# Kernel optimization log

Hardware: AMD Instinct MI355X
Metric: run time of the kernel (lower is better)

The kernel has to match this reference:

```python
import jax, jax.numpy as jnp
import numpy as np

OUT_FEATURES = 11008
IN_FEATURES = 4096
GROUP_SIZE = 128
N_GROUPS = IN_FEATURES // GROUP_SIZE


def setup_inputs() -> dict:
    key = jax.random.key(0)
    k1, k2, k3 = jax.random.split(key, 3)
    x = jax.random.normal(k1, (4, 2048, IN_FEATURES), dtype=jnp.float32)
    # random packed bytes: every uint8 pattern decodes to a valid (low, high) nibble pair
    weight_packed = jax.random.randint(k2, (OUT_FEATURES, IN_FEATURES // 2), 0, 256, dtype=jnp.int32)
    # positive per-group scales (typical magnitude ~ max|w|/7)
    scales = jax.random.uniform(k3, (OUT_FEATURES, N_GROUPS), dtype=jnp.float32, minval=1e-3, maxval=0.05)
    return {"x": x, "weight_packed": weight_packed, "scales": scales}


def _dequant(weight_packed, scales):
    # unpack nibbles: low nibble = even index, high nibble = odd index; stored as (q+8)
    even = (weight_packed & 15) - 8                    # [O, I/2]
    odd = ((weight_packed >> 4) & 15) - 8              # [O, I/2]
    w_q = jnp.stack([even, odd], axis=-1).reshape(OUT_FEATURES, IN_FEATURES)  # interleave
    w = w_q.astype(jnp.float32).reshape(OUT_FEATURES, N_GROUPS, GROUP_SIZE)
    w = w * scales[:, :, None]                          # group-wise dequant
    return w.reshape(OUT_FEATURES, IN_FEATURES)


def reference(x, weight_packed, scales):
    w = _dequant(weight_packed, scales).astype(x.dtype)  # [O, I]
    # F.linear(x, w) = x @ w.T
    return jnp.einsum('bsi,oi->bso', x, w)
```

## Files before the change

### kernel.cpp

```cpp
#include <hip/hip_runtime.h>
#include <stdint.h>

#define K_DIM 4096
#define N_GROUPS 32

#define BM 128
#define BN 128
#define BK 32

typedef __attribute__((ext_vector_type(4))) float f32x4;
typedef __attribute__((ext_vector_type(8))) __bf16 bf16x8;

__device__ __forceinline__ unsigned short f2bf(float f) {
    union { float f; unsigned u; } c; c.f = f;
    unsigned u = c.u;
    u += 0x7FFFu + ((u >> 16) & 1u);
    return (unsigned short)(u >> 16);
}

__global__ __launch_bounds__(256) void cvt_x(const float* __restrict__ x,
                                             unsigned short* __restrict__ xb,
                                             int total) {
    int i = (blockIdx.x * 256 + threadIdx.x) * 8;
    if (i >= total) return;
    f32x4 a = *(const f32x4*)(x + i);
    f32x4 b = *(const f32x4*)(x + i + 4);
    union { unsigned short u[8]; uint4 v; } o;
    o.u[0] = f2bf(a.x); o.u[1] = f2bf(a.y); o.u[2] = f2bf(a.z); o.u[3] = f2bf(a.w);
    o.u[4] = f2bf(b.x); o.u[5] = f2bf(b.y); o.u[6] = f2bf(b.z); o.u[7] = f2bf(b.w);
    *(uint4*)(xb + i) = o.v;
}

__global__ __launch_bounds__(256) void dequant_w(const int* __restrict__ wp,
                                                 const float* __restrict__ sc,
                                                 unsigned short* __restrict__ wd,
                                                 int total4) {
    int idx = blockIdx.x * 256 + threadIdx.x;
    if (idx >= total4) return;
    const int4 v = ((const int4*)wp)[idx];
    int flat = idx << 2;
    int n = flat >> 11;
    int ci = flat & 2047;
    float s = sc[(n << 5) + (ci >> 6)];
    union { unsigned short u[8]; uint4 q; } o;
    int vv[4] = { v.x, v.y, v.z, v.w };
#pragma unroll
    for (int j = 0; j < 4; ++j) {
        int e = (vv[j] & 15) - 8;
        int d = ((vv[j] >> 4) & 15) - 8;
        o.u[2 * j]     = f2bf((float)e * s);
        o.u[2 * j + 1] = f2bf((float)d * s);
    }
    *(uint4*)(wd + ((size_t)n << 12) + (ci << 1)) = o.q;
}

__device__ __forceinline__ void gld16(const void* g, void* l) {
    __builtin_amdgcn_global_load_lds((__attribute__((address_space(1))) void*)g,
                                     (__attribute__((address_space(3))) void*)l,
                                     16, 0, 0);
}

__global__ __launch_bounds__(256, 2) void gemm_bt(const unsigned short* __restrict__ A,
                                                  const unsigned short* __restrict__ B,
                                                  float* __restrict__ C,
                                                  int M, int N) {
    __shared__ __align__(16) unsigned short As[2][BM * BK];
    __shared__ __align__(16) unsigned short Bs[2][BN * BK];

    const int tid  = threadIdx.x;
    const int wave = tid >> 6;
    const int lane = tid & 63;

    const int ntn = N / BN;
    const int G = 16;
    const int bpg = G * ntn;
    const int bid = blockIdx.x;
    const int g   = bid / bpg;
    const int r   = bid % bpg;
    const int tm  = g * G + (r & (G - 1));
    const int tn  = r >> 4;

    const int m0 = tm * BM;
    const int n0 = tn * BN;
    const int wm = (wave >> 1) * 64;
    const int wn = (wave & 1) * 64;

    const int srow = wave * 32 + (lane >> 2);
    const int scol = (lane & 3) * 8;
    const unsigned short* ag = A + (size_t)(m0 + srow) * K_DIM + scol;
    const unsigned short* bg = B + (size_t)(n0 + srow) * K_DIM + scol;
    const int lbase = wave * 1024;

    const int fr = lane & 15;
    const int fk = (lane >> 4) * 8;

    f32x4 acc[4][4] = {};

    gld16(ag, As[0] + lbase);
    gld16(ag + (size_t)16 * K_DIM, As[0] + lbase + 512);
    gld16(bg, Bs[0] + lbase);
    gld16(bg + (size_t)16 * K_DIM, Bs[0] + lbase + 512);

    int buf = 0;
    for (int k0 = 0; k0 < K_DIM; k0 += BK, buf ^= 1) {
        __syncthreads();

        if (k0 + BK < K_DIM) {
            const int kn = k0 + BK;
            unsigned short* al = As[buf ^ 1] + lbase;
            unsigned short* bl = Bs[buf ^ 1] + lbase;
            gld16(ag + kn, al);
            gld16(ag + kn + (size_t)16 * K_DIM, al + 512);
            gld16(bg + kn, bl);
            gld16(bg + kn + (size_t)16 * K_DIM, bl + 512);
        }

        const unsigned short* Ab = As[buf];
        const unsigned short* Bb = Bs[buf];
        bf16x8 af[4], bf[4];
#pragma unroll
        for (int i = 0; i < 4; ++i) {
            af[i] = *(const bf16x8*)(Ab + (wm + i * 16 + fr) * BK + fk);
            bf[i] = *(const bf16x8*)(Bb + (wn + i * 16 + fr) * BK + fk);
        }
#pragma unroll
        for (int i = 0; i < 4; ++i)
#pragma unroll
            for (int j = 0; j < 4; ++j)
                acc[i][j] = __builtin_amdgcn_mfma_f32_16x16x32_bf16(af[i], bf[j], acc[i][j], 0, 0, 0);
    }

    const int cr = (lane >> 4) * 4;
    const int cc = lane & 15;
#pragma unroll
    for (int i = 0; i < 4; ++i) {
#pragma unroll
        for (int j = 0; j < 4; ++j) {
            float* cp = C + (size_t)(m0 + wm + i * 16 + cr) * N + (n0 + wn + j * 16 + cc);
            cp[0]            = acc[i][j].x;
            cp[(size_t)N]    = acc[i][j].y;
            cp[(size_t)N*2]  = acc[i][j].z;
            cp[(size_t)N*3]  = acc[i][j].w;
        }
    }
}

__global__ __launch_bounds__(256, 2) void fused_gemm(const float* __restrict__ X,
                                                     const int* __restrict__ Wp,
                                                     const float* __restrict__ Sc,
                                                     float* __restrict__ C,
                                                     int M, int N) {
    __shared__ __align__(16) unsigned short As[BM * BK];
    __shared__ __align__(16) unsigned short Bs[BN * BK];

    const int tid  = threadIdx.x;
    const int wave = tid >> 6;
    const int lane = tid & 63;
    const int m0 = blockIdx.y * BM;
    const int n0 = blockIdx.x * BN;
    const int wm = (wave >> 1) * 64;
    const int wn = (wave & 1) * 64;

    const int fr = lane & 15;
    const int fk = (lane >> 4) * 8;

    f32x4 acc[4][4] = {};

    for (int k0 = 0; k0 < K_DIM; k0 += BK) {
        __syncthreads();
#pragma unroll
        for (int j = 0; j < 4; ++j) {
            int f = tid + 256 * j;
            int row = f >> 3, c4 = f & 7;
            f32x4 a = *(const f32x4*)(X + (size_t)(m0 + row) * K_DIM + k0 + c4 * 4);
            union { unsigned short u[4]; uint2 q; } o;
            o.u[0] = f2bf(a.x); o.u[1] = f2bf(a.y); o.u[2] = f2bf(a.z); o.u[3] = f2bf(a.w);
            *(uint2*)(As + row * BK + c4 * 4) = o.q;
        }
#pragma unroll
        for (int j = 0; j < 2; ++j) {
            int g = tid + 256 * j;
            int row = g >> 2, c4 = g & 3;
            const int4 v = *(const int4*)(Wp + (size_t)(n0 + row) * (K_DIM / 2) + (k0 >> 1) + c4 * 4);
            float s = Sc[(n0 + row) * N_GROUPS + (k0 >> 7)];
            union { unsigned short u[8]; uint4 q; } o;
            int vv[4] = { v.x, v.y, v.z, v.w };
#pragma unroll
            for (int t = 0; t < 4; ++t) {
                o.u[2 * t]     = f2bf((float)((vv[t] & 15) - 8) * s);
                o.u[2 * t + 1] = f2bf((float)(((vv[t] >> 4) & 15) - 8) * s);
            }
            *(uint4*)(Bs + row * BK + c4 * 8) = o.q;
        }
        __syncthreads();

        bf16x8 af[4], bf[4];
#pragma unroll
        for (int i = 0; i < 4; ++i) {
            af[i] = *(const bf16x8*)(As + (wm + i * 16 + fr) * BK + fk);
            bf[i] = *(const bf16x8*)(Bs + (wn + i * 16 + fr) * BK + fk);
        }
#pragma unroll
        for (int i = 0; i < 4; ++i)
#pragma unroll
            for (int j = 0; j < 4; ++j)
                acc[i][j] = __builtin_amdgcn_mfma_f32_16x16x32_bf16(af[i], bf[j], acc[i][j], 0, 0, 0);
    }

    const int cr = (lane >> 4) * 4;
    const int cc = lane & 15;
#pragma unroll
    for (int i = 0; i < 4; ++i) {
#pragma unroll
        for (int j = 0; j < 4; ++j) {
            float* cp = C + (size_t)(m0 + wm + i * 16 + cr) * N + (n0 + wn + j * 16 + cc);
            cp[0]           = acc[i][j].x;
            cp[(size_t)N]   = acc[i][j].y;
            cp[(size_t)N*2] = acc[i][j].z;
            cp[(size_t)N*3] = acc[i][j].w;
        }
    }
}

extern "C" void kernel_launch(void* const* d_in, const int* in_sizes, int n_in,
                              void* d_out, int out_size, void* d_ws, size_t ws_size,
                              hipStream_t stream) {
    const float* x  = (const float*)d_in[0];
    const int*   wp = (const int*)d_in[1];
    const float* sc = (const float*)d_in[2];
    float* out = (float*)d_out;

    const int M = in_sizes[0] / K_DIM;
    const int N = in_sizes[2] / N_GROUPS;

    const size_t xb_bytes = (size_t)M * K_DIM * 2;
    const size_t wd_bytes = (size_t)N * K_DIM * 2;

    if (ws_size >= xb_bytes + wd_bytes) {
        unsigned short* xb = (unsigned short*)d_ws;
        unsigned short* wd = (unsigned short*)((char*)d_ws + xb_bytes);
        int xtot = M * K_DIM;
        cvt_x<<<xtot / (256 * 8), 256, 0, stream>>>(x, xb, xtot);
        int wtot4 = N * (K_DIM / 2) / 4;
        dequant_w<<<(wtot4 + 255) / 256, 256, 0, stream>>>(wp, sc, wd, wtot4);
        gemm_bt<<<(M / BM) * (N / BN), 256, 0, stream>>>(xb, wd, out, M, N);
    } else {
        dim3 grid(N / BN, M / BM);
        fused_gemm<<<grid, 256, 0, stream>>>(x, wp, sc, out, M, N);
    }
}
```

Measured before the change: 1.313 ms.

## Replace bf16 GEMM with 256x256 eight-wave pipelined kernel with swizzled LDS

```diff
diff --git a/kernel.cpp b/kernel.cpp
--- a/kernel.cpp
+++ b/kernel.cpp
@@ -8,8 +8,14 @@
 #define BN 128
 #define BK 32
 
+#define BM8 256
+#define BN8 256
+#define BK8 64
+#define NT8 (K_DIM / BK8)
+
 typedef __attribute__((ext_vector_type(4))) float f32x4;
 typedef __attribute__((ext_vector_type(8))) __bf16 bf16x8;
+typedef __attribute__((ext_vector_type(4))) unsigned int u32x4;
 
 __device__ __forceinline__ unsigned short f2bf(float f) {
     union { float f; unsigned u; } c; c.f = f;
@@ -60,87 +66,158 @@
                                      16, 0, 0);
 }
 
-__global__ __launch_bounds__(256, 2) void gemm_bt(const unsigned short* __restrict__ A,
-                                                  const unsigned short* __restrict__ B,
-                                                  float* __restrict__ C,
-                                                  int M, int N) {
-    __shared__ __align__(16) unsigned short As[2][BM * BK];
-    __shared__ __align__(16) unsigned short Bs[2][BN * BK];
+__device__ __forceinline__ bf16x8 dsr(unsigned a) {
+    u32x4 d;
+    asm volatile("ds_read_b128 %0, %1" : "=v"(d) : "v"(a));
+    union { u32x4 u; bf16x8 b; } c; c.u = d;
+    return c.b;
+}
+
+__device__ __forceinline__ unsigned lds_addr(const void* p) {
+    return (unsigned)(uintptr_t)(__attribute__((address_space(3))) const void*)p;
+}
+
+#define MFMA_(va, vb, vc) __builtin_amdgcn_mfma_f32_16x16x32_bf16(va, vb, vc, 0, 0, 0)
+
+#define STAGE(regbase, g, k) do {                                   \
+    gld16((g) + (k), (regbase));                                    \
+    gld16((g) + (size_t)128 * K_DIM + (k), (regbase) + 4096); } while (0)
+
+__global__ __launch_bounds__(512, 2) void gemm8p(const unsigned short* __restrict__ A,
+                                                 const unsigned short* __restrict__ B,
+                                                 float* __restrict__ C,
+                                                 int M, int N) {
+    __shared__ __align__(16) unsigned short lds[2][4][8192];
 
     const int tid  = threadIdx.x;
     const int wave = tid >> 6;
     const int lane = tid & 63;
-
-    const int ntn = N / BN;
-    const int G = 16;
-    const int bpg = G * ntn;
+    const int wm = wave >> 2;
+    const int wn = wave & 3;
+
+    const int nwg = gridDim.x;
     const int bid = blockIdx.x;
-    const int g   = bid / bpg;
-    const int r   = bid % bpg;
-    const int tm  = g * G + (r & (G - 1));
-    const int tn  = r >> 4;
-
-    const int m0 = tm * BM;
-    const int n0 = tn * BN;
-    const int wm = (wave >> 1) * 64;
-    const int wn = (wave & 1) * 64;
-
-    const int srow = wave * 32 + (lane >> 2);
-    const int scol = (lane & 3) * 8;
-    const unsigned short* ag = A + (size_t)(m0 + srow) * K_DIM + scol;
-    const unsigned short* bg = B + (size_t)(n0 + srow) * K_DIM + scol;
-    const int lbase = wave * 1024;
+    const int q = nwg >> 3, r7 = nwg & 7;
+    const int xcd = bid & 7, loc = bid >> 3;
+    const int tile = (xcd < r7 ? xcd * (q + 1) : r7 * (q + 1) + (xcd - r7) * q) + loc;
+    const int ntm = M / BM8;
+    const int tm = tile % ntm;
+    const int tn = tile / ntm;
+    const int m0 = tm * BM8;
+    const int n0 = tn * BN8;
+
+    const int srow = lane >> 2;
+    const int sx   = ((lane & 3) * 8) ^ (((lane >> 3) & 3) << 3);
+    const unsigned short* Ag = A + (size_t)(m0 + wave * 16 + srow) * K_DIM + sx;
+    const unsigned short* Bg = B + (size_t)(n0 + wave * 16 + srow) * K_DIM + sx;
+    unsigned short* L  = &lds[0][0][0];
+    unsigned short* Ld = L + wave * 512;
 
     const int fr = lane & 15;
-    const int fk = (lane >> 4) * 8;
-
-    f32x4 acc[4][4] = {};
-
-    gld16(ag, As[0] + lbase);
-    gld16(ag + (size_t)16 * K_DIM, As[0] + lbase + 512);
-    gld16(bg, Bs[0] + lbase);
-    gld16(bg + (size_t)16 * K_DIM, Bs[0] + lbase + 512);
-
-    int buf = 0;
-    for (int k0 = 0; k0 < K_DIM; k0 += BK, buf ^= 1) {
-        __syncthreads();
-
-        if (k0 + BK < K_DIM) {
-            const int kn = k0 + BK;
-            unsigned short* al = As[buf ^ 1] + lbase;
-            unsigned short* bl = Bs[buf ^ 1] + lbase;
-            gld16(ag + kn, al);
-            gld16(ag + kn + (size_t)16 * K_DIM, al + 512);
-            gld16(bg + kn, bl);
-            gld16(bg + kn + (size_t)16 * K_DIM, bl + 512);
-        }
-
-        const unsigned short* Ab = As[buf];
-        const unsigned short* Bb = Bs[buf];
-        bf16x8 af[4], bf[4];
-#pragma unroll
-        for (int i = 0; i < 4; ++i) {
-            af[i] = *(const bf16x8*)(Ab + (wm + i * 16 + fr) * BK + fk);
-            bf[i] = *(const bf16x8*)(Bb + (wn + i * 16 + fr) * BK + fk);
-        }
-#pragma unroll
-        for (int i = 0; i < 4; ++i)
-#pragma unroll
-            for (int j = 0; j < 4; ++j)
-                acc[i][j] = __builtin_amdgcn_mfma_f32_16x16x32_bf16(af[i], bf[j], acc[i][j], 0, 0, 0);
+    const unsigned rofs = (unsigned)(fr * 64 + (((lane >> 4) * 16) ^ (((fr >> 1) & 3) << 4)));
+    const unsigned ldsb = lds_addr(L);
+    const unsigned aoff = ldsb + (unsigned)(wm * 8192) + rofs;
+    const unsigned boff = ldsb + 32768u + (unsigned)(wn * 4096) + rofs;
+
+    f32x4 acc[8][4] = {};
+    bf16x8 a0[4], a1[4], b0[4], b1[4];
+
+    STAGE(Ld + 0 * 8192, Ag, 0);
+    STAGE(Ld + 1 * 8192, Ag, 32);
+    STAGE(Ld + 2 * 8192, Bg, 0);
+    STAGE(Ld + 3 * 8192, Bg, 32);
+    STAGE(Ld + 32768 + 2 * 8192, Bg, 64);
+    STAGE(Ld + 32768 + 0 * 8192, Ag, 64);
+    STAGE(Ld + 32768 + 3 * 8192, Bg, 96);
+    asm volatile("s_waitcnt vmcnt(6)" ::: "memory");
+    __builtin_amdgcn_s_barrier();
+
+    for (int T = 0; T < NT8; ++T) {
+        const int buf = T & 1;
+        const unsigned ab = aoff + (unsigned)(buf * 65536);
+        const unsigned bb = boff + (unsigned)(buf * 65536);
+        unsigned short* Lc = Ld + buf * 32768;
+        unsigned short* Ln = Ld + (buf ^ 1) * 32768;
+        const int kn1 = ((T + 1) < NT8 ? (T + 1) : NT8 - 1) * BK8;
+        const int kn2 = ((T + 2) < NT8 ? (T + 2) : NT8 - 1) * BK8;
+
+#pragma unroll
+        for (int i = 0; i < 4; ++i) a0[i] = dsr(ab + i * 1024u);
+#pragma unroll
+        for (int j = 0; j < 4; ++j) b0[j] = dsr(bb + j * 1024u);
+        STAGE(Ln + 1 * 8192, Ag, kn1 + 32);
+        __builtin_amdgcn_s_barrier();
+        asm volatile("s_waitcnt lgkmcnt(0)" ::: "memory");
+        __builtin_amdgcn_sched_barrier(0);
+        __builtin_amdgcn_s_setprio(1);
+#pragma unroll
+        for (int i = 0; i < 4; ++i)
+#pragma unroll
+            for (int j = 0; j < 4; ++j)
+                acc[i][j] = MFMA_(a0[i], b0[j], acc[i][j]);
+        __builtin_amdgcn_s_setprio(0);
+        __builtin_amdgcn_s_barrier();
+
+#pragma unroll
+        for (int i = 0; i < 4; ++i) a1[i] = dsr(ab + (4 + i) * 1024u);
+        STAGE(Lc + 2 * 8192, Bg, kn2);
+        __builtin_amdgcn_s_barrier();
+        asm volatile("s_waitcnt lgkmcnt(0)" ::: "memory");
+        __builtin_amdgcn_sched_barrier(0);
+        __builtin_amdgcn_s_setprio(1);
+#pragma unroll
+        for (int i = 0; i < 4; ++i)
+#pragma unroll
+            for (int j = 0; j < 4; ++j)
+                acc[4 + i][j] = MFMA_(a1[i], b0[j], acc[4 + i][j]);
+        __builtin_amdgcn_s_setprio(0);
+        __builtin_amdgcn_s_barrier();
+
+#pragma unroll
+        for (int i = 0; i < 4; ++i) a0[i] = dsr(ab + 16384u + i * 1024u);
+#pragma unroll
+        for (int j = 0; j < 4; ++j) b1[j] = dsr(bb + 16384u + j * 1024u);
+        STAGE(Lc + 0 * 8192, Ag, kn2);
+        __builtin_amdgcn_s_barrier();
+        asm volatile("s_waitcnt lgkmcnt(0)" ::: "memory");
+        __builtin_amdgcn_sched_barrier(0);
+        __builtin_amdgcn_s_setprio(1);
+#pragma unroll
+        for (int i = 0; i < 4; ++i)
+#pragma unroll
+            for (int j = 0; j < 4; ++j)
+                acc[i][j] = MFMA_(a0[i], b1[j], acc[i][j]);
+        __builtin_amdgcn_s_setprio(0);
+        __builtin_amdgcn_s_barrier();
+
+#pragma unroll
+        for (int i = 0; i < 4; ++i) a1[i] = dsr(ab + 16384u + (4 + i) * 1024u);
+        STAGE(Lc + 3 * 8192, Bg, kn2 + 32);
+        __builtin_amdgcn_s_barrier();
+        asm volatile("s_waitcnt lgkmcnt(0)" ::: "memory");
+        __builtin_amdgcn_sched_barrier(0);
+        __builtin_amdgcn_s_setprio(1);
+#pragma unroll
+        for (int i = 0; i < 4; ++i)
+#pragma unroll
+            for (int j = 0; j < 4; ++j)
+                acc[4 + i][j] = MFMA_(a1[i], b1[j], acc[4 + i][j]);
+        __builtin_amdgcn_s_setprio(0);
+        asm volatile("s_waitcnt vmcnt(6)" ::: "memory");
+        __builtin_amdgcn_s_barrier();
     }
 
     const int cr = (lane >> 4) * 4;
     const int cc = lane & 15;
 #pragma unroll
-    for (int i = 0; i < 4; ++i) {
+    for (int i = 0; i < 8; ++i) {
 #pragma unroll
         for (int j = 0; j < 4; ++j) {
-            float* cp = C + (size_t)(m0 + wm + i * 16 + cr) * N + (n0 + wn + j * 16 + cc);
-            cp[0]            = acc[i][j].x;
-            cp[(size_t)N]    = acc[i][j].y;
-            cp[(size_t)N*2]  = acc[i][j].z;
-            cp[(size_t)N*3]  = acc[i][j].w;
+            float* cp = C + (size_t)(m0 + wm * 128 + i * 16 + cr) * N + (n0 + wn * 64 + j * 16 + cc);
+            cp[0]           = acc[i][j].x;
+            cp[(size_t)N]   = acc[i][j].y;
+            cp[(size_t)N*2] = acc[i][j].z;
+            cp[(size_t)N*3] = acc[i][j].w;
         }
     }
 }
@@ -236,14 +313,16 @@
     const size_t xb_bytes = (size_t)M * K_DIM * 2;
     const size_t wd_bytes = (size_t)N * K_DIM * 2;
 
-    if (ws_size >= xb_bytes + wd_bytes) {
+    const bool div256 = (M % BM8 == 0) && (N % BN8 == 0);
+
+    if (ws_size >= xb_bytes + wd_bytes && div256) {
         unsigned short* xb = (unsigned short*)d_ws;
         unsigned short* wd = (unsigned short*)((char*)d_ws + xb_bytes);
         int xtot = M * K_DIM;
         cvt_x<<<xtot / (256 * 8), 256, 0, stream>>>(x, xb, xtot);
         int wtot4 = N * (K_DIM / 2) / 4;
         dequant_w<<<(wtot4 + 255) / 256, 256, 0, stream>>>(wp, sc, wd, wtot4);
-        gemm_bt<<<(M / BM) * (N / BN), 256, 0, stream>>>(xb, wd, out, M, N);
+        gemm8p<<<(M / BM8) * (N / BN8), 512, 0, stream>>>(xb, wd, out, M, N);
     } else {
         dim3 grid(N / BN, M / BM);
         fused_gemm<<<grid, 256, 0, stream>>>(x, wp, sc, out, M, N);
```

Result: faster. 1.238 ms (-5.7%).
